# Performance work log

Hardware: AMD Instinct MI355X
Metric: run time of the kernel (lower is better)

## Reference

```python
import jax, jax.numpy as jnp
import numpy as np

B, C, H, W = 16, 64, 32, 32

def conv1x1(x, w, b=None):
    # x: [b,c,h,w], w: [o,c]
    y = jnp.einsum('bchw,oc->bohw', x, w)
    return y if b is None else y + b[None, :, None, None]

def bn(x, s, b, eps=1e-5):
    # training-mode batchnorm over (N,H,W)
    m = x.mean(axis=(0, 2, 3), keepdims=True)
    v = x.var(axis=(0, 2, 3), keepdims=True)
    return (x - m) * jax.lax.rsqrt(v + eps) * s[None, :, None, None] + b[None, :, None, None]

def block(x, w1, s1, b1, w2, s2, b2, ws=None, ss=None, bs=None):
    # BasicBlock with k1=k2=1, stride 1
    y = jax.nn.relu(bn(conv1x1(x, w1), s1, b1))
    y = bn(conv1x1(y, w2), s2, b2)
    sc = x if ws is None else bn(conv1x1(x, ws), ss, bs)
    return jax.nn.relu(y + sc)

def setup_inputs():
    key = jax.random.key(0)
    ks = iter(jax.random.split(key, 32))
    def wmat(o, i):
        return jax.random.normal(next(ks), (o, i), jnp.float32) * 0.05
    d = {}
    d['xa'] = jax.random.normal(next(ks), (B, C, H, W), jnp.float32)
    d['xb'] = jax.random.normal(next(ks), (B, C, H, W), jnp.float32)
    for n in ['qa', 'qb', 'ka', 'kb']:
        d['w' + n] = wmat(C, C)
        d['b' + n] = jnp.zeros((C,), jnp.float32)
    for blk, cin, cout in [('a1', 2 * C, 2 * C), ('b1', 2 * C, 2 * C), ('a2', 2 * C, 4 * C), ('b2', 2 * C, 4 * C)]:
        d[blk + '_w1'] = wmat(cout, cin)
        d[blk + '_s1'] = jnp.ones((cout,), jnp.float32)
        d[blk + '_b1'] = jnp.zeros((cout,), jnp.float32)
        d[blk + '_w2'] = wmat(cout, cout)
        d[blk + '_s2'] = jnp.ones((cout,), jnp.float32)
        d[blk + '_b2'] = jnp.zeros((cout,), jnp.float32)
        if cin != cout:
            d[blk + '_ws'] = wmat(cout, cin)
            d[blk + '_ss'] = jnp.ones((cout,), jnp.float32)
            d[blk + '_bs'] = jnp.zeros((cout,), jnp.float32)
    for o in ['oa', 'ob']:
        d[o + '_w'] = wmat(C, 4 * C)
        d[o + '_s'] = jnp.ones((C,), jnp.float32)
        d[o + '_b'] = jnp.zeros((C,), jnp.float32)
    return d

def reference(xa, xb, wqa, bqa, wqb, bqb, wka, bka, wkb, bkb,
              a1_w1, a1_s1, a1_b1, a1_w2, a1_s2, a1_b2,
              b1_w1, b1_s1, b1_b1, b1_w2, b1_s2, b1_b2,
              a2_w1, a2_s1, a2_b1, a2_w2, a2_s2, a2_b2, a2_ws, a2_ss, a2_bs,
              b2_w1, b2_s1, b2_b1, b2_w2, b2_s2, b2_b2, b2_ws, b2_ss, b2_bs,
              oa_w, oa_s, oa_b, ob_w, ob_s, ob_b):
    b, c = xa.shape[0], xa.shape[1]
    qa = conv1x1(xa, wqa, bqa).reshape(b, c, -1)   # [b,c,na]
    qb = conv1x1(xb, wqb, bqb).reshape(b, c, -1)   # [b,c,nb]
    energy = jnp.einsum('bci,bcj->bij', qa, qb)    # [b,na,nb]
    flat = energy.reshape(b, -1)
    m = jnp.max(flat, axis=-1, keepdims=True)
    # DANet-style: softmax over the FULL flattened na*nb axis of (max - energy)
    att = jax.nn.softmax(m - flat, axis=-1).reshape(energy.shape)
    ka = conv1x1(xa, wka, bka).reshape(b, c, -1)
    kb = conv1x1(xb, wkb, bkb).reshape(b, c, -1)
    xb_att = jnp.einsum('bij,bcj->bci', att, kb).reshape(xa.shape)
    xa_att = jnp.einsum('bij,bci->bcj', att, ka).reshape(xb.shape)
    ya = jnp.concatenate([xa, xb_att], axis=1)
    yb = jnp.concatenate([xb, xa_att], axis=1)
    ya = block(ya, a1_w1, a1_s1, a1_b1, a1_w2, a1_s2, a1_b2)
    ya = block(ya, a2_w1, a2_s1, a2_b1, a2_w2, a2_s2, a2_b2, a2_ws, a2_ss, a2_bs)
    yb = block(yb, b1_w1, b1_s1, b1_b1, b1_w2, b1_s2, b1_b2)
    yb = block(yb, b2_w1, b2_s1, b2_b1, b2_w2, b2_s2, b2_b2, b2_ws, b2_ss, b2_bs)
    ya = bn(conv1x1(ya, oa_w), oa_s, oa_b)
    yb = bn(conv1x1(yb, ob_w), ob_s, ob_b)
    return (ya, yb)
```

## Files before the change

kernel.cpp:

```cpp
#include <hip/hip_runtime.h>
#include <hip/hip_bf16.h>
#include <cstddef>

static constexpr int BATCH = 16;
static constexpr int NCOPY = 16;
static constexpr int SSTR  = NCOPY * 512;

typedef __attribute__((ext_vector_type(8))) short bf16x8;
typedef __attribute__((ext_vector_type(4))) float f32x4;

__device__ __forceinline__ unsigned short f2bf(float f) {
  unsigned u = __float_as_uint(f);
  return (unsigned short)((u + 0x7fffu + ((u >> 16) & 1u)) >> 16);
}

#define SEL4(dst, arr, idx)                                   \
  do {                                                        \
    if ((idx) == 0) dst = arr[0];                             \
    else if ((idx) == 1) dst = arr[1];                        \
    else if ((idx) == 2) dst = arr[2];                        \
    else dst = arr[3];                                        \
  } while (0)

__global__ void init_kernel(float* __restrict__ t, int n) {
  int i = blockIdx.x * 256 + threadIdx.x;
  if (i < n) t[i] = 0.f;
}

struct WcvtArgs { const float* p[16]; int sz[16]; int off[16]; };
__global__ __launch_bounds__(256)
void wcvt_kernel(WcvtArgs a, unsigned short* __restrict__ dst) {
  const int t = blockIdx.x;
  const float* src = a.p[t];
  unsigned short* d = dst + a.off[t];
  const int sz = a.sz[t];
  for (int i = blockIdx.y * 256 + threadIdx.x; i < sz; i += 16 * 256)
    d[i] = f2bf(src[i]);
}

__global__ __launch_bounds__(256)
void xcvt_kernel(const float* __restrict__ XA, const float* __restrict__ XB,
                 unsigned short* __restrict__ XAt, unsigned short* __restrict__ XBt) {
  __shared__ float ts[64][66];
  const int tid = threadIdx.x;
  const int n0 = blockIdx.x << 6;
  const int b = blockIdx.y;
  const int z = blockIdx.z;
  const float* X = z ? XB : XA;
  unsigned short* XT = z ? XBt : XAt;
#pragma unroll
  for (int it = 0; it < 4; ++it) {
    int idx = it * 256 + tid;
    int c = idx >> 4, nq = (idx & 15) << 2;
    float4 v = *reinterpret_cast<const float4*>(X + ((size_t)(b * 64 + c) << 10) + n0 + nq);
    ts[c][nq] = v.x; ts[c][nq + 1] = v.y; ts[c][nq + 2] = v.z; ts[c][nq + 3] = v.w;
  }
  __syncthreads();
  const int n = tid >> 2, c0 = (tid & 3) << 4;
  unsigned short* dst = XT + ((size_t)(b * 1024 + n0 + n) << 6) + c0;
  unsigned w0 = (unsigned)f2bf(ts[c0 + 0][n]) | ((unsigned)f2bf(ts[c0 + 1][n]) << 16);
  unsigned w1 = (unsigned)f2bf(ts[c0 + 2][n]) | ((unsigned)f2bf(ts[c0 + 3][n]) << 16);
  unsigned w2 = (unsigned)f2bf(ts[c0 + 4][n]) | ((unsigned)f2bf(ts[c0 + 5][n]) << 16);
  unsigned w3 = (unsigned)f2bf(ts[c0 + 6][n]) | ((unsigned)f2bf(ts[c0 + 7][n]) << 16);
  unsigned w4 = (unsigned)f2bf(ts[c0 + 8][n]) | ((unsigned)f2bf(ts[c0 + 9][n]) << 16);
  unsigned w5 = (unsigned)f2bf(ts[c0 + 10][n]) | ((unsigned)f2bf(ts[c0 + 11][n]) << 16);
  unsigned w6 = (unsigned)f2bf(ts[c0 + 12][n]) | ((unsigned)f2bf(ts[c0 + 13][n]) << 16);
  unsigned w7 = (unsigned)f2bf(ts[c0 + 14][n]) | ((unsigned)f2bf(ts[c0 + 15][n]) << 16);
  *reinterpret_cast<uint4*>(dst) = make_uint4(w0, w1, w2, w3);
  *reinterpret_cast<uint4*>(dst + 8) = make_uint4(w4, w5, w6, w7);
}

struct QBias { const float* p[4]; };
__global__ __launch_bounds__(256, 4)
void qk_mfma_kernel(const unsigned short* __restrict__ XAt,
                    const unsigned short* __restrict__ XBt,
                    const unsigned short* __restrict__ wq,
                    QBias qb,
                    unsigned short* __restrict__ QAt, unsigned short* __restrict__ QBt,
                    unsigned short* __restrict__ KAc, unsigned short* __restrict__ KBc) {
  __shared__ __align__(16) unsigned char Xs[64 * 128];
  const int tid = threadIdx.x;
  const int lane = tid & 63, w = tid >> 6;
  const int g = lane >> 4, m = lane & 15;
  const int nbase = blockIdx.x << 6;
  const int z = blockIdx.y;
  const int which = z >> 4;
  const int b = z & 15;
  const unsigned short* XT = (which & 1) ? XBt : XAt;
  const unsigned short* Wb = wq + which * 4096;
  const float* bias;
  SEL4(bias, qb.p, which);
#pragma unroll
  for (int it = 0; it < 2; ++it) {
    int idx = it * 256 + tid;
    int row = idx >> 3, cc = idx & 7;
    bf16x8 v = *reinterpret_cast<const bf16x8*>(
        XT + ((size_t)(b * 1024 + nbase + row) << 6) + cc * 8);
    const int byte = (cc << 4) ^ ((row & 7) << 4);
    *reinterpret_cast<bf16x8*>(Xs + row * 128 + byte) = v;
  }
  __syncthreads();
  const int o0 = w << 4;
  const unsigned short* Wr = Wb + (size_t)(o0 + m) * 64 + (g << 3);
  bf16x8 af0 = *reinterpret_cast<const bf16x8*>(Wr);
  bf16x8 af1 = *reinterpret_cast<const bf16x8*>(Wr + 32);
  float bv[4];
#pragma unroll
  for (int r = 0; r < 4; ++r) bv[r] = bias[o0 + (g << 2) + r];
#pragma unroll
  for (int nt = 0; nt < 4; ++nt) {
    const int row = (nt << 4) + m;
    const unsigned char* lrow = Xs + row * 128;
    const int swz = (row & 7) << 4;
    f32x4 acc = (f32x4){0.f, 0.f, 0.f, 0.f};
    {
      bf16x8 b0 = *reinterpret_cast<const bf16x8*>(lrow + ((g << 4) ^ swz));
      acc = __builtin_amdgcn_mfma_f32_16x16x32_bf16(af0, b0, acc, 0, 0, 0);
      bf16x8 b1 = *reinterpret_cast<const bf16x8*>(lrow + ((64 + (g << 4)) ^ swz));
      acc = __builtin_amdgcn_mfma_f32_16x16x32_bf16(af1, b1, acc, 0, 0, 0);
    }
#pragma unroll
    for (int r = 0; r < 4; ++r) acc[r] += bv[r];
    if (which < 2) {
      unsigned short* Yq = (which == 0) ? QAt : QBt;
      ushort4 v;
      v.x = f2bf(acc[0]); v.y = f2bf(acc[1]);
      v.z = f2bf(acc[2]); v.w = f2bf(acc[3]);
      *reinterpret_cast<ushort4*>(
          Yq + ((size_t)(b * 1024 + nbase + row) << 6) + o0 + (g << 2)) = v;
    } else {
      unsigned short* Kc = (which == 2) ? KAc : KBc;
#pragma unroll
      for (int r = 0; r < 4; ++r)
        Kc[((size_t)b << 16) + ((size_t)(o0 + (g << 2) + r) << 10) + nbase + row] =
            f2bf(acc[r]);
    }
  }
}

__global__ __launch_bounds__(256)
void attn_mfma_kernel(const unsigned short* __restrict__ QAt,
                      const unsigned short* __restrict__ QBt,
                      const unsigned short* __restrict__ KAc,
                      const unsigned short* __restrict__ KBc,
                      float* __restrict__ PART, float* __restrict__ bsum) {
  __shared__ __align__(16) unsigned short Ua[4096];
  __shared__ __align__(16) unsigned short Vb[4096];
  __shared__ __align__(16) unsigned short Pl[4096];
  __shared__ float red[256];
  const int tid = threadIdx.x;
  const int lane = tid & 63, w = tid >> 6;
  const int g = lane >> 4, m = lane & 15;
  const int z = blockIdx.z;
  const bool isPV = (z < 16);
  const int b = z & 15;
  const size_t nb = (size_t)b << 16;
  const size_t M1 = (size_t)1 << 20;

  if (isPV) {
    const int i0 = blockIdx.x << 6;
    const int jbase = blockIdx.y << 9;
    {
      const unsigned short* src = QAt + nb + ((size_t)i0 << 6);
#pragma unroll
      for (int s = 0; s < 2; ++s) {
        int idx = tid + (s << 8);
        int n = idx >> 3, cc = idx & 7;
        bf16x8 v = *reinterpret_cast<const bf16x8*>(src + (n << 6) + ((cc ^ (n & 7)) << 3));
        *reinterpret_cast<bf16x8*>(Ua + (idx << 3)) = v;
      }
    }
    f32x4 accO[4];
#pragma unroll
    for (int n = 0; n < 4; ++n) accO[n] = (f32x4){0.f, 0.f, 0.f, 0.f};
    float psum = 0.f;
    for (int jt = 0; jt < 8; ++jt) {
      const int j0 = jbase + (jt << 6);
      __syncthreads();
      {
        const unsigned short* src = QBt + nb + ((size_t)j0 << 6);
#pragma unroll
        for (int s = 0; s < 2; ++s) {
          int idx = tid + (s << 8);
          int n = idx >> 3, cc = idx & 7;
          bf16x8 v = *reinterpret_cast<const bf16x8*>(src + (n << 6) + ((cc ^ (n & 7)) << 3));
          *reinterpret_cast<bf16x8*>(Vb + (idx << 3)) = v;
        }
      }
      __syncthreads();
      const int jrow = (w << 4) | m;
      bf16x8 a0 = *reinterpret_cast<const bf16x8*>(Vb + (jrow << 6) + ((g ^ (jrow & 7)) << 3));
      bf16x8 a1 = *reinterpret_cast<const bf16x8*>(Vb + (jrow << 6) + (((g + 4) ^ (jrow & 7)) << 3));
      f32x4 e[4];
#pragma unroll
      for (int n = 0; n < 4; ++n) {
        const int irow = (n << 4) | m;
        bf16x8 b0v = *reinterpret_cast<const bf16x8*>(Ua + (irow << 6) + ((g ^ (irow & 7)) << 3));
        bf16x8 b1v = *reinterpret_cast<const bf16x8*>(Ua + (irow << 6) + (((g + 4) ^ (irow & 7)) << 3));
        e[n] = (f32x4){0.f, 0.f, 0.f, 0.f};
        e[n] = __builtin_amdgcn_mfma_f32_16x16x32_bf16(a0, b0v, e[n], 0, 0, 0);
        e[n] = __builtin_amdgcn_mfma_f32_16x16x32_bf16(a1, b1v, e[n], 0, 0, 0);
      }
      const int j = (w << 4) | (g << 2);
#pragma unroll
      for (int n = 0; n < 4; ++n) {
        const int irow = (n << 4) | m;
        float p0 = __expf(-e[n][0]), p1 = __expf(-e[n][1]);
        float p2 = __expf(-e[n][2]), p3 = __expf(-e[n][3]);
        psum += (p0 + p1) + (p2 + p3);
        unsigned pk01 = (unsigned)f2bf(p0) | ((unsigned)f2bf(p1) << 16);
        unsigned pk23 = (unsigned)f2bf(p2) | ((unsigned)f2bf(p3) << 16);
        int base = irow << 6;
        int off0 = base + ((((j) >> 3) ^ (irow & 7)) << 3) + (j & 7);
        int off2 = base + ((((j + 2) >> 3) ^ (irow & 7)) << 3) + ((j + 2) & 7);
        *reinterpret_cast<unsigned*>(Pl + off0) = pk01;
        *reinterpret_cast<unsigned*>(Pl + off2) = pk23;
      }
      const int crow = (w << 4) | m;
      const unsigned short* kbp = KBc + nb + ((size_t)crow << 10) + j0 + (g << 3);
      bf16x8 ka0 = *reinterpret_cast<const bf16x8*>(kbp);
      bf16x8 ka1 = *reinterpret_cast<const bf16x8*>(kbp + 32);
      __syncthreads();
#pragma unroll
      for (int n = 0; n < 4; ++n) {
        const int irow = (n << 4) | m;
        bf16x8 p0 = *reinterpret_cast<const bf16x8*>(Pl + (irow << 6) + ((g ^ (irow & 7)) << 3));
        bf16x8 p1 = *reinterpret_cast<const bf16x8*>(Pl + (irow << 6) + (((g + 4) ^ (irow & 7)) << 3));
        accO[n] = __builtin_amdgcn_mfma_f32_16x16x32_bf16(ka0, p0, accO[n], 0, 0, 0);
        accO[n] = __builtin_amdgcn_mfma_f32_16x16x32_bf16(ka1, p1, accO[n], 0, 0, 0);
      }
    }
    float* OUT = PART + ((size_t)blockIdx.y * M1) + ((size_t)(b * 64) << 10);
#pragma unroll
    for (int n = 0; n < 4; ++n) {
      const int ig = i0 + (n << 4) + m;
      const int c = (w << 4) + (g << 2);
#pragma unroll
      for (int r = 0; r < 4; ++r)
        OUT[((size_t)(c + r) << 10) + ig] = accO[n][r];
    }
    red[tid] = psum; __syncthreads();
    for (int s = 128; s > 0; s >>= 1) {
      if (tid < s) red[tid] += red[tid + s];
      __syncthreads();
    }
    if (tid == 0) atomicAdd(bsum + b, red[0]);
  } else {
    const int j0 = blockIdx.x << 6;
    const int ibase = blockIdx.y << 9;
    {
      const unsigned short* src = QBt + nb + ((size_t)j0 << 6);
#pragma unroll
      for (int s = 0; s < 2; ++s) {
        int idx = tid + (s << 8);
        int n = idx >> 3, cc = idx & 7;
        bf16x8 v = *reinterpret_cast<const bf16x8*>(src + (n << 6) + ((cc ^ (n & 7)) << 3));
        *reinterpret_cast<bf16x8*>(Ua + (idx << 3)) = v;
      }
    }
    f32x4 accO[4];
#pragma unroll
    for (int n = 0; n < 4; ++n) accO[n] = (f32x4){0.f, 0.f, 0.f, 0.f};
    for (int it = 0; it < 8; ++it) {
      const int i0 = ibase + (it << 6);
      __syncthreads();
      {
        const unsigned short* src = QAt + nb + ((size_t)i0 << 6);
#pragma unroll
        for (int s = 0; s < 2; ++s) {
          int idx = tid + (s << 8);
          int n = idx >> 3, cc = idx & 7;
          bf16x8 v = *reinterpret_cast<const bf16x8*>(src + (n << 6) + ((cc ^ (n & 7)) << 3));
          *reinterpret_cast<bf16x8*>(Vb + (idx << 3)) = v;
        }
      }
      __syncthreads();
      const int irow_a = (w << 4) | m;
      bf16x8 a0 = *reinterpret_cast<const bf16x8*>(Vb + (irow_a << 6) + ((g ^ (irow_a & 7)) << 3));
      bf16x8 a1 = *reinterpret_cast<const bf16x8*>(Vb + (irow_a << 6) + (((g + 4) ^ (irow_a & 7)) << 3));
      f32x4 e[4];
#pragma unroll
      for (int n = 0; n < 4; ++n) {
        const int jrow = (n << 4) | m;
        bf16x8 b0v = *reinterpret_cast<const bf16x8*>(Ua + (jrow << 6) + ((g ^ (jrow & 7)) << 3));
        bf16x8 b1v = *reinterpret_cast<const bf16x8*>(Ua + (jrow << 6) + (((g + 4) ^ (jrow & 7)) << 3));
        e[n] = (f32x4){0.f, 0.f, 0.f, 0.f};
        e[n] = __builtin_amdgcn_mfma_f32_16x16x32_bf16(a0, b0v, e[n], 0, 0, 0);
        e[n] = __builtin_amdgcn_mfma_f32_16x16x32_bf16(a1, b1v, e[n], 0, 0, 0);
      }
      const int i = (w << 4) | (g << 2);
#pragma unroll
      for (int n = 0; n < 4; ++n) {
        const int jrow = (n << 4) | m;
        float p0 = __expf(-e[n][0]), p1 = __expf(-e[n][1]);
        float p2 = __expf(-e[n][2]), p3 = __expf(-e[n][3]);
        unsigned pk01 = (unsigned)f2bf(p0) | ((unsigned)f2bf(p1) << 16);
        unsigned pk23 = (unsigned)f2bf(p2) | ((unsigned)f2bf(p3) << 16);
        int base = jrow << 6;
        int off0 = base + ((((i) >> 3) ^ (jrow & 7)) << 3) + (i & 7);
        int off2 = base + ((((i + 2) >> 3) ^ (jrow & 7)) << 3) + ((i + 2) & 7);
        *reinterpret_cast<unsigned*>(Pl + off0) = pk01;
        *reinterpret_cast<unsigned*>(Pl + off2) = pk23;
      }
      const int crow = (w << 4) | m;
      const unsigned short* kap = KAc + nb + ((size_t)crow << 10) + i0 + (g << 3);
      bf16x8 ka0 = *reinterpret_cast<const bf16x8*>(kap);
      bf16x8 ka1 = *reinterpret_cast<const bf16x8*>(kap + 32);
      __syncthreads();
#pragma unroll
      for (int n = 0; n < 4; ++n) {
        const int jrow = (n << 4) | m;
        bf16x8 p0 = *reinterpret_cast<const bf16x8*>(Pl + (jrow << 6) + ((g ^ (jrow & 7)) << 3));
        bf16x8 p1 = *reinterpret_cast<const bf16x8*>(Pl + (jrow << 6) + (((g + 4) ^ (jrow & 7)) << 3));
        accO[n] = __builtin_amdgcn_mfma_f32_16x16x32_bf16(ka0, p0, accO[n], 0, 0, 0);
        accO[n] = __builtin_amdgcn_mfma_f32_16x16x32_bf16(ka1, p1, accO[n], 0, 0, 0);
      }
    }
    float* OUT = PART + 2 * M1 + ((size_t)blockIdx.y * M1) + ((size_t)(b * 64) << 10);
#pragma unroll
    for (int n = 0; n < 4; ++n) {
      const int jg = j0 + (n << 4) + m;
      const int c = (w << 4) + (g << 2);
#pragma unroll
      for (int r = 0; r < 4; ++r)
        OUT[((size_t)(c + r) << 10) + jg] = accO[n][r];
    }
  }
}

__global__ __launch_bounds__(256)
void merge_kernel(const float* __restrict__ PARTb, const float* __restrict__ XA,
                  const float* __restrict__ XB, unsigned short* __restrict__ Y0b,
                  const float* __restrict__ bsum) {
  __shared__ float ts[128][66];
  const int tid = threadIdx.x;
  const int n0 = blockIdx.x << 6;
  const int b = blockIdx.y;
  const int z = blockIdx.z;
  const float invS = 1.f / bsum[b];
  const size_t M1 = (size_t)1 << 20;
  const float* XR = z ? XB : XA;
  const float* PART = PARTb + (size_t)z * 2 * M1;
  unsigned short* Y0 = Y0b + (size_t)z * 2 * M1;
#pragma unroll
  for (int it = 0; it < 4; ++it) {
    int idx = it * 256 + tid;
    int c = idx >> 4, nq = (idx & 15) << 2;
    float4 v = *reinterpret_cast<const float4*>(XR + ((size_t)(b * 64 + c) << 10) + n0 + nq);
    ts[c][nq] = v.x; ts[c][nq + 1] = v.y; ts[c][nq + 2] = v.z; ts[c][nq + 3] = v.w;
  }
#pragma unroll
  for (int it = 0; it < 4; ++it) {
    int idx = it * 256 + tid;
    int c = idx >> 4, nq = (idx & 15) << 2;
    const float* p = PART + ((size_t)(b * 64 + c) << 10) + n0 + nq;
    float4 av = *reinterpret_cast<const float4*>(p);
    float4 b4 = *reinterpret_cast<const float4*>(p + M1);
    ts[64 + c][nq]     = (av.x + b4.x) * invS;
    ts[64 + c][nq + 1] = (av.y + b4.y) * invS;
    ts[64 + c][nq + 2] = (av.z + b4.z) * invS;
    ts[64 + c][nq + 3] = (av.w + b4.w) * invS;
  }
  __syncthreads();
  const int n = tid >> 2, c0 = (tid & 3) << 5;
  unsigned short* dst = Y0 + ((size_t)(b * 1024 + n0 + n) << 7) + c0;
#pragma unroll
  for (int q8 = 0; q8 < 4; ++q8) {
    const int cb = c0 + (q8 << 3);
    unsigned w0 = (unsigned)f2bf(ts[cb + 0][n]) | ((unsigned)f2bf(ts[cb + 1][n]) << 16);
    unsigned w1 = (unsigned)f2bf(ts[cb + 2][n]) | ((unsigned)f2bf(ts[cb + 3][n]) << 16);
    unsigned w2 = (unsigned)f2bf(ts[cb + 4][n]) | ((unsigned)f2bf(ts[cb + 5][n]) << 16);
    unsigned w3 = (unsigned)f2bf(ts[cb + 6][n]) | ((unsigned)f2bf(ts[cb + 7][n]) << 16);
    *reinterpret_cast<uint4*>(dst + (q8 << 3)) = make_uint4(w0, w1, w2, w3);
  }
}

struct GBArgs { const float* g0[4]; const float* b0[4];
                const float* g1[4]; const float* b1[4]; };

template<int CIN, int OC, int SMODE, int XDIV>
__global__ __launch_bounds__(256, 4)
void conv_mfma_kernel(const unsigned short* __restrict__ T0,
                      const unsigned short* __restrict__ S0,
                      const unsigned short* __restrict__ W0,
                      unsigned short* __restrict__ Yout0,
                      const float* __restrict__ sums0A, long s0str,
                      const float* __restrict__ sums1A, long s1str,
                      GBArgs gb,
                      float* __restrict__ outSums0,
                      int COUT, long tstr, long sstr, long wstr, long ystr) {
  constexpr int KS = CIN / 32;
  constexpr int ROWB = CIN * 2;
  constexpr int CPR = CIN / 8;
  __shared__ __align__(16) unsigned char Xs[64 * ROWB];
  __shared__ float scs[(SMODE >= 1) ? CIN : 1];
  __shared__ float shs[(SMODE >= 1) ? CIN : 1];
  __shared__ float sc2[(SMODE == 3) ? CIN : 1];
  __shared__ float sh2[(SMODE == 3) ? CIN : 1];
  const int tid = threadIdx.x;
  const int lane = tid & 63, w = tid >> 6;
  const int g = lane >> 4, m = lane & 15;
  const int z = blockIdx.z;
  const int zi = z >> XDIV;
  const int obase = blockIdx.x * (OC << 6) + (w << 4);
  const int nbase = blockIdx.y << 6;
  const unsigned short* Tin = T0 + (size_t)zi * tstr;
  const unsigned short* Sin = (SMODE >= 2) ? (S0 + (size_t)zi * sstr) : nullptr;
  const unsigned short* Wb  = W0 + (size_t)z * wstr;
  unsigned short* Yout      = Yout0 + (size_t)z * ystr;
  float* outSums            = outSums0 + (size_t)z * SSTR;
  if (SMODE >= 1) {
    const float* s0 = sums0A + (size_t)zi * s0str;
    const float* gg0; const float* bb0;
    SEL4(gg0, gb.g0, zi); SEL4(bb0, gb.b0, zi);
    const float invN = 1.f / 16384.f;
    for (int c = tid; c < CIN; c += 256) {
      float ss = 0.f, qq = 0.f;
#pragma unroll
      for (int p = 0; p < NCOPY; ++p) {
        ss += s0[p * 512 + c];
        qq += s0[p * 512 + 256 + c];
      }
      float mm = ss * invN;
      float vv = qq * invN - mm * mm;
      float s = gg0[c] * rsqrtf(vv + 1e-5f);
      scs[c] = s; shs[c] = bb0[c] - mm * s;
    }
    if (SMODE == 3) {
      const float* s1 = sums1A + (size_t)zi * s1str;
      const float* gg1; const float* bb1;
      SEL4(gg1, gb.g1, zi); SEL4(bb1, gb.b1, zi);
      for (int c = tid; c < CIN; c += 256) {
        float ss = 0.f, qq = 0.f;
#pragma unroll
        for (int p = 0; p < NCOPY; ++p) {
          ss += s1[p * 512 + c];
          qq += s1[p * 512 + 256 + c];
        }
        float mm = ss * invN;
        float vv = qq * invN - mm * mm;
        float s = gg1[c] * rsqrtf(vv + 1e-5f);
        sc2[c] = s; sh2[c] = bb1[c] - mm * s;
      }
    }
    __syncthreads();
  }
#pragma unroll
  for (int it = 0; it < (64 * CPR) / 256; ++it) {
    const int idx = it * 256 + tid;
    const int row = idx / CPR;
    const int cc = idx % CPR;
    bf16x8 v = *reinterpret_cast<const bf16x8*>(
        Tin + (size_t)(nbase + row) * CIN + cc * 8);
    if (SMODE >= 1) {
      bf16x8 sv;
      if (SMODE >= 2)
        sv = *reinterpret_cast<const bf16x8*>(
            Sin + (size_t)(nbase + row) * CIN + cc * 8);
      const int c0 = cc * 8;
#pragma unroll
      for (int j = 0; j < 8; ++j) {
        float x = __uint_as_float((unsigned)(unsigned short)v[j] << 16);
        x = fmaf(x, scs[c0 + j], shs[c0 + j]);
        if (SMODE == 2)
          x += __uint_as_float((unsigned)(unsigned short)sv[j] << 16);
        if (SMODE == 3) {
          float y = __uint_as_float((unsigned)(unsigned short)sv[j] << 16);
          x += fmaf(y, sc2[c0 + j], sh2[c0 + j]);
        }
        x = fmaxf(x, 0.f);
        v[j] = (short)f2bf(x);
      }
    }
    const int byte = (cc << 4) ^ ((row & 7) << 4);
    *reinterpret_cast<bf16x8*>(Xs + row * ROWB + byte) = v;
  }
  __syncthreads();
  bf16x8 af[KS][OC];
#pragma unroll
  for (int oc = 0; oc < OC; ++oc) {
    const unsigned short* Wr = Wb + (size_t)(obase + (oc << 6) + m) * CIN + (g << 3);
#pragma unroll
    for (int k = 0; k < KS; ++k)
      af[k][oc] = *reinterpret_cast<const bf16x8*>(Wr + (k << 5));
  }
  float sr[OC][4], qr[OC][4];
#pragma unroll
  for (int oc = 0; oc < OC; ++oc)
#pragma unroll
    for (int r = 0; r < 4; ++r) { sr[oc][r] = 0.f; qr[oc][r] = 0.f; }
#pragma unroll
  for (int nt = 0; nt < 4; ++nt) {
    const int row = (nt << 4) + m;
    const unsigned char* lrow = Xs + row * ROWB;
    const int swz = (row & 7) << 4;
    f32x4 acc[OC];
#pragma unroll
    for (int oc = 0; oc < OC; ++oc) acc[oc] = (f32x4){0.f, 0.f, 0.f, 0.f};
#pragma unroll
    for (int k = 0; k < KS; ++k) {
      const int byte = ((k << 6) + (g << 4)) ^ swz;
      bf16x8 bv = *reinterpret_cast<const bf16x8*>(lrow + byte);
#pragma unroll
      for (int oc = 0; oc < OC; ++oc)
        acc[oc] = __builtin_amdgcn_mfma_f32_16x16x32_bf16(af[k][oc], bv, acc[oc], 0, 0, 0);
    }
#pragma unroll
    for (int oc = 0; oc < OC; ++oc) {
      ushort4 v;
      v.x = f2bf(acc[oc][0]); v.y = f2bf(acc[oc][1]);
      v.z = f2bf(acc[oc][2]); v.w = f2bf(acc[oc][3]);
      *reinterpret_cast<ushort4*>(
          Yout + (size_t)(nbase + row) * COUT + obase + (oc << 6) + (g << 2)) = v;
#pragma unroll
      for (int r = 0; r < 4; ++r) {
        sr[oc][r] += acc[oc][r];
        qr[oc][r] = fmaf(acc[oc][r], acc[oc][r], qr[oc][r]);
      }
    }
  }
#pragma unroll
  for (int oc = 0; oc < OC; ++oc)
#pragma unroll
    for (int r = 0; r < 4; ++r) {
      for (int off = 1; off < 16; off <<= 1) {
        sr[oc][r] += __shfl_xor(sr[oc][r], off);
        qr[oc][r] += __shfl_xor(qr[oc][r], off);
      }
    }
  if (m == 0) {
    float* dst = outSums + (blockIdx.y & (NCOPY - 1)) * 512;
#pragma unroll
    for (int oc = 0; oc < OC; ++oc)
#pragma unroll
      for (int r = 0; r < 4; ++r) {
        atomicAdd(&dst[obase + (oc << 6) + (g << 2) + r], sr[oc][r]);
        atomicAdd(&dst[256 + obase + (oc << 6) + (g << 2) + r], qr[oc][r]);
      }
  }
}

__global__ __launch_bounds__(256)
void writeout_t_kernel(const unsigned short* __restrict__ F0,
                       const float* __restrict__ sumsA,
                       GBArgs gb,
                       float* __restrict__ out0) {
  __shared__ float ts[64][66];
  __shared__ float sc[64], sh[64];
  const int tid = threadIdx.x;
  const int z = blockIdx.z;
  const size_t M1 = (size_t)1 << 20;
  const unsigned short* F = F0 + (size_t)z * M1;
  float* outp = out0 + (size_t)z * M1;
  if (tid < 64) {
    const float* sums = sumsA + (size_t)z * SSTR;
    const float* gg; const float* bb;
    SEL4(gg, gb.g0, z); SEL4(bb, gb.b0, z);
    float s0 = 0.f, q0 = 0.f;
#pragma unroll
    for (int p = 0; p < NCOPY; ++p) {
      s0 += sums[p * 512 + tid];
      q0 += sums[p * 512 + 256 + tid];
    }
    const float invN = 1.f / 16384.f;
    float mm = s0 * invN;
    float vv = q0 * invN - mm * mm;
    float s = gg[tid] * rsqrtf(vv + 1e-5f);
    sc[tid] = s; sh[tid] = bb[tid] - mm * s;
  }
  __syncthreads();
  const int n0 = blockIdx.x << 6;
  const int b = blockIdx.y;
  {
    const int n = tid >> 2, c0 = (tid & 3) << 4;
    const unsigned short* Fr = F + ((size_t)(b * 1024 + n0 + n) << 6) + c0;
    uint4 v0 = *reinterpret_cast<const uint4*>(Fr);
    uint4 v1 = *reinterpret_cast<const uint4*>(Fr + 8);
    unsigned vw[8] = {v0.x, v0.y, v0.z, v0.w, v1.x, v1.y, v1.z, v1.w};
#pragma unroll
    for (int jw = 0; jw < 8; ++jw) {
      int c = c0 + jw * 2;
      float x0 = __uint_as_float((vw[jw] & 0xffffu) << 16);
      float x1 = __uint_as_float((vw[jw] >> 16) << 16);
      ts[c][n] = fmaf(x0, sc[c], sh[c]);
      ts[c + 1][n] = fmaf(x1, sc[c + 1], sh[c + 1]);
    }
  }
  __syncthreads();
  const int c = tid >> 2, nq = (tid & 3) << 4;
  float* orow = outp + ((size_t)(b * 64 + c) << 10) + n0 + nq;
#pragma unroll
  for (int q = 0; q < 4; ++q) {
    float4 ov;
    ov.x = ts[c][nq + q * 4 + 0]; ov.y = ts[c][nq + q * 4 + 1];
    ov.z = ts[c][nq + q * 4 + 2]; ov.w = ts[c][nq + q * 4 + 3];
    *reinterpret_cast<float4*>(orow + q * 4) = ov;
  }
}

extern "C" void kernel_launch(void* const* d_in, const int* in_sizes, int n_in,
                              void* d_out, int out_size, void* d_ws, size_t ws_size,
                              hipStream_t stream) {
  float* wsf = (float*)d_ws;
  const size_t M1 = (size_t)1 << 20;
  const size_t H1 = (size_t)1 << 19;

  unsigned short* QAt = (unsigned short*)wsf;
  unsigned short* QBt = (unsigned short*)(wsf + H1);
  unsigned short* KAc = (unsigned short*)(wsf + 2 * H1);
  unsigned short* KBc = (unsigned short*)(wsf + 3 * H1);
  float* PART1 = wsf + 2 * M1;
  unsigned short* XAt = (unsigned short*)(wsf + 6 * M1);
  unsigned short* XBt = (unsigned short*)(wsf + 7 * M1);
  unsigned short* Y0A = (unsigned short*)(wsf + 10 * M1);
  unsigned short* T1a = (unsigned short*)(wsf + 12 * M1);
  unsigned short* T2a = (unsigned short*)(wsf + 14 * M1);
  unsigned short* T3a = (unsigned short*)(wsf + 18 * M1);
  unsigned short* T4a = (unsigned short*)(wsf + 26 * M1);
  unsigned short* Fba = (unsigned short*)(wsf + 30 * M1);
  float* tail = wsf + 31 * M1;
  float* bsum = tail;
  float* stats = tail + 16;
  unsigned short* wbf = (unsigned short*)(stats + 12 * SSTR);

  const float* pp[46];
  for (int i = 0; i < 46 && i < n_in; ++i) pp[i] = (const float*)d_in[i];

  const int initN = 16 + 12 * SSTR;
  init_kernel<<<(initN + 255) / 256, 256, 0, stream>>>(tail, initN);

  const int widx[16] = {2, 4, 6, 8,
                        10, 16, 13, 19, 22, 28, 31, 37, 25, 34, 40, 43};
  WcvtArgs wa;
  int woff[16];
  {
    int run = 0;
    for (int i = 0; i < 16; ++i) {
      wa.p[i] = pp[widx[i]];
      wa.sz[i] = in_sizes[widx[i]];
      wa.off[i] = run; woff[i] = run;
      run += in_sizes[widx[i]];
    }
  }
  wcvt_kernel<<<dim3(16, 16), 256, 0, stream>>>(wa, wbf);

  xcvt_kernel<<<dim3(16, BATCH, 2), 256, 0, stream>>>(pp[0], pp[1], XAt, XBt);

  QBias qb;
  qb.p[0] = pp[3]; qb.p[1] = pp[5]; qb.p[2] = pp[7]; qb.p[3] = pp[9];
  qk_mfma_kernel<<<dim3(16, 64), 256, 0, stream>>>(
      XAt, XBt, wbf + woff[0], qb, QAt, QBt, KAc, KBc);

  attn_mfma_kernel<<<dim3(16, 2, 32), 256, 0, stream>>>(
      QAt, QBt, KAc, KBc, PART1, bsum);
  merge_kernel<<<dim3(16, BATCH, 2), 256, 0, stream>>>(PART1, pp[0], pp[1], Y0A, bsum);

  float* S_c1 = stats;
  float* S_c2 = stats + 2 * SSTR;
  float* S_q  = stats + 4 * SSTR;
  float* S_c4 = stats + 8 * SSTR;
  float* S_c6 = stats + 10 * SSTR;

  const long SH1 = (long)2 * M1;
  const long SH2 = (long)4 * M1;
  GBArgs gbE = {};
  GBArgs gb;

  conv_mfma_kernel<128, 2, 0, 0><<<dim3(1, 256, 2), 256, 0, stream>>>(
      Y0A, nullptr, wbf + woff[4], T1a, nullptr, 0, nullptr, 0, gbE,
      S_c1, 128, SH1, 0, 16384, SH1);

  gb = gbE;
  gb.g0[0] = pp[11]; gb.b0[0] = pp[12]; gb.g0[1] = pp[17]; gb.b0[1] = pp[18];
  conv_mfma_kernel<128, 2, 1, 0><<<dim3(1, 256, 2), 256, 0, stream>>>(
      T1a, nullptr, wbf + woff[6], T2a, S_c1, SSTR, nullptr, 0, gb,
      S_c2, 128, SH1, 0, 16384, SH1);

  gb = gbE;
  gb.g0[0] = pp[14]; gb.b0[0] = pp[15]; gb.g0[1] = pp[20]; gb.b0[1] = pp[21];
  conv_mfma_kernel<128, 2, 2, 1><<<dim3(2, 256, 4), 256, 0, stream>>>(
      T2a, Y0A, wbf + woff[8], T3a, S_c2, SSTR, nullptr, 0, gb,
      S_q, 256, SH1, SH1, 32768, SH2);

  gb = gbE;
  gb.g0[0] = pp[23]; gb.b0[0] = pp[24]; gb.g0[1] = pp[32]; gb.b0[1] = pp[33];
  conv_mfma_kernel<256, 2, 1, 0><<<dim3(2, 256, 2), 256, 0, stream>>>(
      T3a, nullptr, wbf + woff[12], T4a, S_q, 2 * SSTR, nullptr, 0, gb,
      S_c4, 256, (long)8 * M1, 0, 65536, SH2);

  gb = gbE;
  gb.g0[0] = pp[26]; gb.b0[0] = pp[27]; gb.g0[1] = pp[35]; gb.b0[1] = pp[36];
  gb.g1[0] = pp[29]; gb.b1[0] = pp[30]; gb.g1[1] = pp[38]; gb.b1[1] = pp[39];
  conv_mfma_kernel<256, 1, 3, 0><<<dim3(1, 256, 2), 256, 0, stream>>>(
      T4a, T3a + SH2 , wbf + woff[14], Fba, S_c4, SSTR,
      S_q + SSTR, 2 * SSTR, gb,
      S_c6, 64, SH2, (long)8 * M1, 16384, (long)M1);

  gb = gbE;
  gb.g0[0] = pp[41]; gb.b0[0] = pp[42]; gb.g0[1] = pp[44]; gb.b0[1] = pp[45];
  writeout_t_kernel<<<dim3(16, BATCH, 2), 256, 0, stream>>>(
      Fba, S_c6, gb, (float*)d_out);
}
```

Before: 148.6 us.

## Fuse attention merge into first conv and store partials channel-last

```diff
diff --git a/kernel.cpp b/kernel.cpp
--- a/kernel.cpp
+++ b/kernel.cpp
@@ -230,14 +230,14 @@
         accO[n] = __builtin_amdgcn_mfma_f32_16x16x32_bf16(ka1, p1, accO[n], 0, 0, 0);
       }
     }
-    float* OUT = PART + ((size_t)blockIdx.y * M1) + ((size_t)(b * 64) << 10);
+    float* OUT = PART + ((size_t)blockIdx.y * M1) + nb;
 #pragma unroll
     for (int n = 0; n < 4; ++n) {
       const int ig = i0 + (n << 4) + m;
       const int c = (w << 4) + (g << 2);
-#pragma unroll
-      for (int r = 0; r < 4; ++r)
-        OUT[((size_t)(c + r) << 10) + ig] = accO[n][r];
+      float4 o;
+      o.x = accO[n][0]; o.y = accO[n][1]; o.z = accO[n][2]; o.w = accO[n][3];
+      *reinterpret_cast<float4*>(OUT + ((size_t)ig << 6) + c) = o;
     }
     red[tid] = psum; __syncthreads();
     for (int s = 128; s > 0; s >>= 1) {
@@ -316,62 +316,15 @@
         accO[n] = __builtin_amdgcn_mfma_f32_16x16x32_bf16(ka1, p1, accO[n], 0, 0, 0);
       }
     }
-    float* OUT = PART + 2 * M1 + ((size_t)blockIdx.y * M1) + ((size_t)(b * 64) << 10);
+    float* OUT = PART + 2 * M1 + ((size_t)blockIdx.y * M1) + nb;
 #pragma unroll
     for (int n = 0; n < 4; ++n) {
       const int jg = j0 + (n << 4) + m;
       const int c = (w << 4) + (g << 2);
-#pragma unroll
-      for (int r = 0; r < 4; ++r)
-        OUT[((size_t)(c + r) << 10) + jg] = accO[n][r];
-    }
-  }
-}
-
-__global__ __launch_bounds__(256)
-void merge_kernel(const float* __restrict__ PARTb, const float* __restrict__ XA,
-                  const float* __restrict__ XB, unsigned short* __restrict__ Y0b,
-                  const float* __restrict__ bsum) {
-  __shared__ float ts[128][66];
-  const int tid = threadIdx.x;
-  const int n0 = blockIdx.x << 6;
-  const int b = blockIdx.y;
-  const int z = blockIdx.z;
-  const float invS = 1.f / bsum[b];
-  const size_t M1 = (size_t)1 << 20;
-  const float* XR = z ? XB : XA;
-  const float* PART = PARTb + (size_t)z * 2 * M1;
-  unsigned short* Y0 = Y0b + (size_t)z * 2 * M1;
-#pragma unroll
-  for (int it = 0; it < 4; ++it) {
-    int idx = it * 256 + tid;
-    int c = idx >> 4, nq = (idx & 15) << 2;
-    float4 v = *reinterpret_cast<const float4*>(XR + ((size_t)(b * 64 + c) << 10) + n0 + nq);
-    ts[c][nq] = v.x; ts[c][nq + 1] = v.y; ts[c][nq + 2] = v.z; ts[c][nq + 3] = v.w;
-  }
-#pragma unroll
-  for (int it = 0; it < 4; ++it) {
-    int idx = it * 256 + tid;
-    int c = idx >> 4, nq = (idx & 15) << 2;
-    const float* p = PART + ((size_t)(b * 64 + c) << 10) + n0 + nq;
-    float4 av = *reinterpret_cast<const float4*>(p);
-    float4 b4 = *reinterpret_cast<const float4*>(p + M1);
-    ts[64 + c][nq]     = (av.x + b4.x) * invS;
-    ts[64 + c][nq + 1] = (av.y + b4.y) * invS;
-    ts[64 + c][nq + 2] = (av.z + b4.z) * invS;
-    ts[64 + c][nq + 3] = (av.w + b4.w) * invS;
-  }
-  __syncthreads();
-  const int n = tid >> 2, c0 = (tid & 3) << 5;
-  unsigned short* dst = Y0 + ((size_t)(b * 1024 + n0 + n) << 7) + c0;
-#pragma unroll
-  for (int q8 = 0; q8 < 4; ++q8) {
-    const int cb = c0 + (q8 << 3);
-    unsigned w0 = (unsigned)f2bf(ts[cb + 0][n]) | ((unsigned)f2bf(ts[cb + 1][n]) << 16);
-    unsigned w1 = (unsigned)f2bf(ts[cb + 2][n]) | ((unsigned)f2bf(ts[cb + 3][n]) << 16);
-    unsigned w2 = (unsigned)f2bf(ts[cb + 4][n]) | ((unsigned)f2bf(ts[cb + 5][n]) << 16);
-    unsigned w3 = (unsigned)f2bf(ts[cb + 6][n]) | ((unsigned)f2bf(ts[cb + 7][n]) << 16);
-    *reinterpret_cast<uint4*>(dst + (q8 << 3)) = make_uint4(w0, w1, w2, w3);
+      float4 o;
+      o.x = accO[n][0]; o.y = accO[n][1]; o.z = accO[n][2]; o.w = accO[n][3];
+      *reinterpret_cast<float4*>(OUT + ((size_t)jg << 6) + c) = o;
+    }
   }
 }
 
@@ -388,13 +341,17 @@
                       const float* __restrict__ sums1A, long s1str,
                       GBArgs gb,
                       float* __restrict__ outSums0,
-                      int COUT, long tstr, long sstr, long wstr, long ystr) {
+                      int COUT, long tstr, long sstr, long wstr, long ystr,
+                      const float* __restrict__ PARTp,
+                      const float* __restrict__ bsumP,
+                      unsigned short* __restrict__ Y0out) {
   constexpr int KS = CIN / 32;
   constexpr int ROWB = CIN * 2;
   constexpr int CPR = CIN / 8;
+  constexpr bool BN0 = (SMODE >= 1 && SMODE <= 3);
   __shared__ __align__(16) unsigned char Xs[64 * ROWB];
-  __shared__ float scs[(SMODE >= 1) ? CIN : 1];
-  __shared__ float shs[(SMODE >= 1) ? CIN : 1];
+  __shared__ float scs[BN0 ? CIN : 1];
+  __shared__ float shs[BN0 ? CIN : 1];
   __shared__ float sc2[(SMODE == 3) ? CIN : 1];
   __shared__ float sh2[(SMODE == 3) ? CIN : 1];
   const int tid = threadIdx.x;
@@ -405,11 +362,11 @@
   const int obase = blockIdx.x * (OC << 6) + (w << 4);
   const int nbase = blockIdx.y << 6;
   const unsigned short* Tin = T0 + (size_t)zi * tstr;
-  const unsigned short* Sin = (SMODE >= 2) ? (S0 + (size_t)zi * sstr) : nullptr;
+  const unsigned short* Sin = (SMODE == 2 || SMODE == 3) ? (S0 + (size_t)zi * sstr) : nullptr;
   const unsigned short* Wb  = W0 + (size_t)z * wstr;
   unsigned short* Yout      = Yout0 + (size_t)z * ystr;
   float* outSums            = outSums0 + (size_t)z * SSTR;
-  if (SMODE >= 1) {
+  if (BN0) {
     const float* s0 = sums0A + (size_t)zi * s0str;
     const float* gg0; const float* bb0;
     SEL4(gg0, gb.g0, zi); SEL4(bb0, gb.b0, zi);
@@ -445,35 +402,70 @@
     }
     __syncthreads();
   }
-#pragma unroll
-  for (int it = 0; it < (64 * CPR) / 256; ++it) {
-    const int idx = it * 256 + tid;
-    const int row = idx / CPR;
-    const int cc = idx % CPR;
-    bf16x8 v = *reinterpret_cast<const bf16x8*>(
-        Tin + (size_t)(nbase + row) * CIN + cc * 8);
-    if (SMODE >= 1) {
-      bf16x8 sv;
-      if (SMODE >= 2)
-        sv = *reinterpret_cast<const bf16x8*>(
-            Sin + (size_t)(nbase + row) * CIN + cc * 8);
-      const int c0 = cc * 8;
-#pragma unroll
-      for (int j = 0; j < 8; ++j) {
-        float x = __uint_as_float((unsigned)(unsigned short)v[j] << 16);
-        x = fmaf(x, scs[c0 + j], shs[c0 + j]);
-        if (SMODE == 2)
-          x += __uint_as_float((unsigned)(unsigned short)sv[j] << 16);
-        if (SMODE == 3) {
-          float y = __uint_as_float((unsigned)(unsigned short)sv[j] << 16);
-          x += fmaf(y, sc2[c0 + j], sh2[c0 + j]);
+  if (SMODE == 4) {
+    const int bb = nbase >> 10;
+    const float invS = 1.f / bsumP[bb];
+    const float* Pz = PARTp + (size_t)zi * ((size_t)2 << 20);
+    unsigned short* Y0o = Y0out + (size_t)zi * ((size_t)2 << 20);
+#pragma unroll
+    for (int it = 0; it < (64 * CPR) / 256; ++it) {
+      const int idx = it * 256 + tid;
+      const int row = idx / CPR;
+      const int cc = idx % CPR;
+      bf16x8 v;
+      if (cc < 8) {
+        v = *reinterpret_cast<const bf16x8*>(
+            Tin + ((size_t)(nbase + row) << 6) + cc * 8);
+      } else {
+        const float* p = Pz + ((size_t)(nbase + row) << 6) + ((cc - 8) << 3);
+        float4 a0 = *reinterpret_cast<const float4*>(p);
+        float4 a1 = *reinterpret_cast<const float4*>(p + 4);
+        float4 b0 = *reinterpret_cast<const float4*>(p + ((size_t)1 << 20));
+        float4 b1 = *reinterpret_cast<const float4*>(p + ((size_t)1 << 20) + 4);
+        v[0] = (short)f2bf((a0.x + b0.x) * invS);
+        v[1] = (short)f2bf((a0.y + b0.y) * invS);
+        v[2] = (short)f2bf((a0.z + b0.z) * invS);
+        v[3] = (short)f2bf((a0.w + b0.w) * invS);
+        v[4] = (short)f2bf((a1.x + b1.x) * invS);
+        v[5] = (short)f2bf((a1.y + b1.y) * invS);
+        v[6] = (short)f2bf((a1.z + b1.z) * invS);
+        v[7] = (short)f2bf((a1.w + b1.w) * invS);
+      }
+      *reinterpret_cast<bf16x8*>(Y0o + (size_t)(nbase + row) * 128 + cc * 8) = v;
+      const int byte = (cc << 4) ^ ((row & 7) << 4);
+      *reinterpret_cast<bf16x8*>(Xs + row * ROWB + byte) = v;
+    }
+  } else {
+#pragma unroll
+    for (int it = 0; it < (64 * CPR) / 256; ++it) {
+      const int idx = it * 256 + tid;
+      const int row = idx / CPR;
+      const int cc = idx % CPR;
+      bf16x8 v = *reinterpret_cast<const bf16x8*>(
+          Tin + (size_t)(nbase + row) * CIN + cc * 8);
+      if (BN0) {
+        bf16x8 sv;
+        if (SMODE >= 2)
+          sv = *reinterpret_cast<const bf16x8*>(
+              Sin + (size_t)(nbase + row) * CIN + cc * 8);
+        const int c0 = cc * 8;
+#pragma unroll
+        for (int j = 0; j < 8; ++j) {
+          float x = __uint_as_float((unsigned)(unsigned short)v[j] << 16);
+          x = fmaf(x, scs[c0 + j], shs[c0 + j]);
+          if (SMODE == 2)
+            x += __uint_as_float((unsigned)(unsigned short)sv[j] << 16);
+          if (SMODE == 3) {
+            float y = __uint_as_float((unsigned)(unsigned short)sv[j] << 16);
+            x += fmaf(y, sc2[c0 + j], sh2[c0 + j]);
+          }
+          x = fmaxf(x, 0.f);
+          v[j] = (short)f2bf(x);
         }
-        x = fmaxf(x, 0.f);
-        v[j] = (short)f2bf(x);
-      }
-    }
-    const int byte = (cc << 4) ^ ((row & 7) << 4);
-    *reinterpret_cast<bf16x8*>(Xs + row * ROWB + byte) = v;
+      }
+      const int byte = (cc << 4) ^ ((row & 7) << 4);
+      *reinterpret_cast<bf16x8*>(Xs + row * ROWB + byte) = v;
+    }
   }
   __syncthreads();
   bf16x8 af[KS][OC];
@@ -653,7 +645,6 @@
 
   attn_mfma_kernel<<<dim3(16, 2, 32), 256, 0, stream>>>(
       QAt, QBt, KAc, KBc, PART1, bsum);
-  merge_kernel<<<dim3(16, BATCH, 2), 256, 0, stream>>>(PART1, pp[0], pp[1], Y0A, bsum);
 
   float* S_c1 = stats;
   float* S_c2 = stats + 2 * SSTR;
@@ -666,27 +657,31 @@
   GBArgs gbE = {};
   GBArgs gb;
 
-  conv_mfma_kernel<128, 2, 0, 0><<<dim3(1, 256, 2), 256, 0, stream>>>(
-      Y0A, nullptr, wbf + woff[4], T1a, nullptr, 0, nullptr, 0, gbE,
-      S_c1, 128, SH1, 0, 16384, SH1);
+  conv_mfma_kernel<128, 2, 4, 0><<<dim3(1, 256, 2), 256, 0, stream>>>(
+      XAt, nullptr, wbf + woff[4], T1a, nullptr, 0, nullptr, 0, gbE,
+      S_c1, 128, SH1, 0, 16384, SH1,
+      PART1, bsum, Y0A);
 
   gb = gbE;
   gb.g0[0] = pp[11]; gb.b0[0] = pp[12]; gb.g0[1] = pp[17]; gb.b0[1] = pp[18];
   conv_mfma_kernel<128, 2, 1, 0><<<dim3(1, 256, 2), 256, 0, stream>>>(
       T1a, nullptr, wbf + woff[6], T2a, S_c1, SSTR, nullptr, 0, gb,
-      S_c2, 128, SH1, 0, 16384, SH1);
+      S_c2, 128, SH1, 0, 16384, SH1,
+      nullptr, nullptr, nullptr);
 
   gb = gbE;
   gb.g0[0] = pp[14]; gb.b0[0] = pp[15]; gb.g0[1] = pp[20]; gb.b0[1] = pp[21];
   conv_mfma_kernel<128, 2, 2, 1><<<dim3(2, 256, 4), 256, 0, stream>>>(
       T2a, Y0A, wbf + woff[8], T3a, S_c2, SSTR, nullptr, 0, gb,
-      S_q, 256, SH1, SH1, 32768, SH2);
+      S_q, 256, SH1, SH1, 32768, SH2,
+      nullptr, nullptr, nullptr);
 
   gb = gbE;
   gb.g0[0] = pp[23]; gb.b0[0] = pp[24]; gb.g0[1] = pp[32]; gb.b0[1] = pp[33];
   conv_mfma_kernel<256, 2, 1, 0><<<dim3(2, 256, 2), 256, 0, stream>>>(
       T3a, nullptr, wbf + woff[12], T4a, S_q, 2 * SSTR, nullptr, 0, gb,
-      S_c4, 256, (long)8 * M1, 0, 65536, SH2);
+      S_c4, 256, (long)8 * M1, 0, 65536, SH2,
+      nullptr, nullptr, nullptr);
 
   gb = gbE;
   gb.g0[0] = pp[26]; gb.b0[0] = pp[27]; gb.g0[1] = pp[35]; gb.b0[1] = pp[36];
@@ -694,7 +689,8 @@
   conv_mfma_kernel<256, 1, 3, 0><<<dim3(1, 256, 2), 256, 0, stream>>>(
       T4a, T3a + SH2 , wbf + woff[14], Fba, S_c4, SSTR,
       S_q + SSTR, 2 * SSTR, gb,
-      S_c6, 64, SH2, (long)8 * M1, 16384, (long)M1);
+      S_c6, 64, SH2, (long)8 * M1, 16384, (long)M1,
+      nullptr, nullptr, nullptr);
 
   gb = gbE;
   gb.g0[0] = pp[41]; gb.b0[0] = pp[42]; gb.g0[1] = pp[44]; gb.b0[1] = pp[45];
```

Result: faster. 144.2 us (-3.0%).
